# Kernel optimization log

Measured on AMD Instinct MI355X. Metric: run time of the kernel, lower is better.

## Reference

```python
import jax, jax.numpy as jnp
import numpy as np

B, N, C, H = 4, 1024, 1024, 16
HD = C // H  # 64
THETA = 10000.0


def _rope_cos_sin(n, hd, theta):
    # classic 1D RoPE cache; [n, hd] with each freq repeated twice (interleaved pairs)
    inv_freq = 1.0 / theta ** (jnp.arange(0, hd, 2, dtype=jnp.float32) / hd)
    t = jnp.arange(n, dtype=jnp.float32)
    freqs = t[:, None] * inv_freq[None, :]              # [n, hd/2]
    cos = jnp.repeat(jnp.cos(freqs), 2, axis=-1)        # [n, hd]
    sin = jnp.repeat(jnp.sin(freqs), 2, axis=-1)
    # original clones & forces row 0 to identity rotation (already true since t=0)
    cos = cos.at[0].set(1.0)
    sin = sin.at[0].set(0.0)
    return cos, sin


def _rotate_half(x):
    # interleaved rotate-half: (x0,x1,x2,x3,...) -> (-x1,x0,-x3,x2,...)
    x1 = x[..., 0::2]
    x2 = x[..., 1::2]
    return jnp.stack((-x2, x1), axis=-1).reshape(x.shape)


def setup_inputs() -> dict:
    key = jax.random.key(0)
    ks = jax.random.split(key, 5)
    s = 0.02
    return {
        "x": jax.random.normal(ks[0], (B, N, C), dtype=jnp.float32),
        "qkv_w": jax.random.normal(ks[1], (3 * C, C), dtype=jnp.float32) * s,
        "qkv_b": jax.random.normal(ks[2], (3 * C,), dtype=jnp.float32) * s,
        "proj_w": jax.random.normal(ks[3], (C, C), dtype=jnp.float32) * s,
        "proj_b": jax.random.normal(ks[4], (C,), dtype=jnp.float32) * s,
    }


def reference(x, qkv_w, qkv_b, proj_w, proj_b):
    b, n, c = x.shape
    h, hd = H, HD
    qkv = x @ qkv_w.T + qkv_b                              # [b, n, 3c]
    qkv = qkv.reshape(b, n, 3, h, hd).transpose(2, 0, 3, 1, 4)  # [3, b, h, n, hd]
    q, k, v = qkv[0], qkv[1], qkv[2]
    scale = hd ** -0.5
    q = q * scale                                          # explicit pre-scale (as in source)
    cos, sin = _rope_cos_sin(n, hd, THETA)                 # [n, hd]
    cos = cos[None, None]                                  # broadcast over b, h
    sin = sin[None, None]
    q = q * cos + _rotate_half(q) * sin
    k = k * cos + _rotate_half(k) * sin
    # F.scaled_dot_product_attention also applies its default 1/sqrt(hd) scale
    logits = jnp.einsum('bhqd,bhkd->bhqk', q, k) * scale   # [b, h, n, n]
    attn = jax.nn.softmax(logits, axis=-1)
    out = jnp.einsum('bhqk,bhkd->bhqd', attn, v)           # [b, h, n, hd]
    out = out.transpose(0, 2, 1, 3).reshape(b, n, c)
    return out @ proj_w.T + proj_b
```

## Files before the change

### kernel.cpp

```cpp
#include <hip/hip_runtime.h>
#include <hip/hip_bf16.h>
#include <stdint.h>

#define DEVI __device__ __forceinline__

typedef __attribute__((ext_vector_type(8))) short short8;
typedef __attribute__((ext_vector_type(4))) short short4v;
typedef __attribute__((ext_vector_type(4))) float floatx4;

DEVI ushort f2bf(float f) {
  union { float f; uint32_t u; } v; v.f = f;
  uint32_t u = v.u;
  uint32_t r = (u + 0x7FFFu + ((u >> 16) & 1u)) >> 16;
  return (ushort)r;
}
DEVI ushort f2bf_fast(float f) {
  union { float f; uint32_t u; } v; v.f = f;
  return (ushort)((v.u + 0x8000u) >> 16);
}
DEVI float bf2f(ushort h) {
  union { uint32_t u; float f; } v; v.u = ((uint32_t)h) << 16;
  return v.f;
}
DEVI void gld_lds16(const void* g, void* l) {
  __builtin_amdgcn_global_load_lds(
      (const __attribute__((address_space(1))) unsigned int*)g,
      (__attribute__((address_space(3))) unsigned int*)l, 16, 0, 0);
}

__global__ __launch_bounds__(256, 4) void cast_all(
    const float* __restrict__ x, const float* __restrict__ w1,
    const float* __restrict__ w2, ushort* __restrict__ xb,
    ushort* __restrict__ w1b, ushort* __restrict__ w2b,
    float2* __restrict__ tab) {
  const int N1 = 4096 * 1024, N2 = 3072 * 1024, N3 = 1024 * 1024;
  int id = blockIdx.x * 256 + threadIdx.x;
  if (id < 32768) {
    int j = id & 31, n = id >> 5;
    float inv = powf(10000.0f, -(float)(2 * j) / 64.0f);
    float fr = (float)n * inv;
    tab[id] = make_float2(cosf(fr), sinf(fr));
  }
  int i = id * 4;
  const int total = N1 + N2 + N3;
  int stride = gridDim.x * 256 * 4;
  for (; i < total; i += stride) {
    const float* src; ushort* dst; int off;
    if (i < N1) { src = x; dst = xb; off = i; }
    else if (i < N1 + N2) { src = w1; dst = w1b; off = i - N1; }
    else { src = w2; dst = w2b; off = i - N1 - N2; }
    float4 v = *(const float4*)(src + off);
    ushort4 o;
    o.x = f2bf(v.x); o.y = f2bf(v.y); o.z = f2bf(v.z); o.w = f2bf(v.w);
    *(ushort4*)(dst + off) = o;
  }
}

__global__ __launch_bounds__(256, 4) void gemm_qkv(
    const ushort* __restrict__ A, const ushort* __restrict__ Bm,
    const float* __restrict__ bias, const float2* __restrict__ tab,
    ushort* __restrict__ Qb, ushort* __restrict__ Kb,
    ushort* __restrict__ Vt) {
  __shared__ __align__(16) char pool[33792];
  char* AsP = pool;
  char* BsP = pool + 16384;
  const int tid = threadIdx.x;
  const int w = tid >> 6, lane = tid & 63;

  const int bid = blockIdx.x;
  const int xcd = bid & 7, i5 = bid >> 3;
  const int lm = i5 & 7, ln = i5 >> 3;
  const int mt = (xcd & 3) * 8 + lm;
  const int nt = (xcd >> 2) * 12 + ln;
  const int m0 = mt * 128, n0 = nt * 128;

  const int wm = (w >> 1) * 64, wn = (w & 1) * 64;
  const int lrow = lane & 15, g = lane >> 4;
  const int swrd = (g ^ ((lrow >> 1) & 3)) << 4;

  const int swsrc = (((lane & 3) ^ ((lane >> 3) & 3)) << 4);
  const char* aG = (const char*)A + (size_t)(m0 + w * 32 + (lane >> 2)) * 2048 + swsrc;
  const char* bG = (const char*)Bm + (size_t)(n0 + w * 32 + (lane >> 2)) * 2048 + swsrc;
  const int ldst = w * 2048 + lane * 16;

  auto STAGE = [&](const int buf) {
    gld_lds16(aG, AsP + buf * 8192 + ldst);
    gld_lds16(aG + 16 * 2048, AsP + buf * 8192 + ldst + 1024);
    gld_lds16(bG, BsP + buf * 8192 + ldst);
    gld_lds16(bG + 16 * 2048, BsP + buf * 8192 + ldst + 1024);
    aG += 64; bG += 64;
  };

  floatx4 acc[4][4] = {};

  auto TILE = [&](const int buf) {
    short8 af[4], bf[4];
#pragma unroll
    for (int t = 0; t < 4; ++t) {
      af[t] = *(const short8*)(AsP + buf * 8192 + (wm + t * 16 + lrow) * 64 + swrd);
      bf[t] = *(const short8*)(BsP + buf * 8192 + (wn + t * 16 + lrow) * 64 + swrd);
    }
#pragma unroll
    for (int i = 0; i < 4; ++i)
#pragma unroll
      for (int j = 0; j < 4; ++j)
        acc[i][j] = __builtin_amdgcn_mfma_f32_16x16x32_bf16(af[i], bf[j], acc[i][j], 0, 0, 0);
  };

  STAGE(0);
  asm volatile("s_waitcnt vmcnt(0)" ::: "memory");
  __builtin_amdgcn_s_barrier();
  __builtin_amdgcn_sched_barrier(0);

  for (int t = 0; t < 32; t += 2) {
    STAGE(1);
    __builtin_amdgcn_sched_barrier(0);
    TILE(0);
    asm volatile("s_waitcnt vmcnt(0)" ::: "memory");
    __builtin_amdgcn_s_barrier();
    __builtin_amdgcn_sched_barrier(0);

    if (t + 2 < 32) STAGE(0);
    __builtin_amdgcn_sched_barrier(0);
    TILE(1);
    asm volatile("s_waitcnt vmcnt(0)" ::: "memory");
    __builtin_amdgcn_s_barrier();
    __builtin_amdgcn_sched_barrier(0);
  }

  const int role = n0 >> 10;
  if (role == 2) {
    char* T = pool;
#pragma unroll
    for (int i = 0; i < 4; ++i) {
      int lr0 = wm + i * 16 + g * 4;
#pragma unroll
      for (int j = 0; j < 4; ++j) {
        int lc = wn + j * 16 + lrow;
        float bv = bias[n0 + lc];
        ushort4 o;
#pragma unroll
        for (int r = 0; r < 4; ++r) ((ushort*)&o)[r] = f2bf(acc[i][j][r] + bv);
        *(ushort4*)(T + lc * 264 + lr0 * 2) = o;
      }
    }
    __syncthreads();
    const int b = m0 >> 10, nbase = m0 & 1023;
    const int h0 = (n0 - 2048) >> 6;
    const int c = tid >> 1, half = tid & 1;
    const int h = h0 + (c >> 6), d = c & 63;
    ushort* dst = Vt + (size_t)(b * 16 + h) * 65536 + (size_t)d * 1024 + nbase + half * 64;
    const char* src = T + c * 264 + half * 128;
#pragma unroll
    for (int k = 0; k < 16; ++k)
      *(short4v*)(dst + k * 4) = *(const short4v*)(src + k * 8);
  } else {
    const float sc = (1.0f / 64.0f) * 1.44269504088896f;
#pragma unroll
    for (int i = 0; i < 4; ++i) {
      int mrow = m0 + wm + i * 16 + g * 4;
#pragma unroll
      for (int j = 0; j < 4; ++j) {
        int ncol = n0 + wn + j * 16 + lrow;
        float bv = bias[ncol];
        int cm = ncol & 1023;
        int h = cm >> 6, d = cm & 63;
#pragma unroll
        for (int r = 0; r < 4; ++r) {
          float v = acc[i][j][r] + bv;
          int row = mrow + r;
          int b = row >> 10, n = row & 1023;
          float p = __shfl_xor(v, 1);
          float2 cs = tab[n * 32 + (d >> 1)];
          float o = (d & 1) ? (v * cs.x + p * cs.y) : (v * cs.x - p * cs.y);
          if (role == 0) o *= sc;
          ushort* dstqk = (role == 0) ? Qb : Kb;
          dstqk[((size_t)(b * 16 + h) * 1024 + n) * 64 + d] = f2bf(o);
        }
      }
    }
  }
}

__global__ __launch_bounds__(256, 3) void gemm_proj(
    const ushort* __restrict__ A, const ushort* __restrict__ Bm,
    const float* __restrict__ bias, float* __restrict__ Cout) {
  __shared__ __align__(16) char lds[3][16384];
  char* L0 = &lds[0][0];
  const int tid = threadIdx.x;
  const int w = tid >> 6, lane = tid & 63;

  const int bid = blockIdx.x;
  const int xcd = bid & 7, i5 = bid >> 3;
  const int lm = i5 & 7, ln = i5 >> 3;
  const int mt = (xcd & 3) * 8 + lm;
  const int nt = (xcd >> 2) * 4 + ln;
  const int m0 = mt * 128, n0 = nt * 128;

  const int wm = (w >> 1) * 64, wn = (w & 1) * 64;
  const int lrow = lane & 15, g = lane >> 4;
  const int swrd = (g ^ ((lrow >> 1) & 3)) << 4;

  const int swsrc = (((lane & 3) ^ ((lane >> 3) & 3)) << 4);
  const char* aG = (const char*)A + (size_t)(m0 + w * 32 + (lane >> 2)) * 2048 + swsrc;
  const char* bG = (const char*)Bm + (size_t)(n0 + w * 32 + (lane >> 2)) * 2048 + swsrc;
  const int ldst = w * 2048 + lane * 16;

  auto STAGE = [&](const int base) {
    char* L = L0 + base;
    gld_lds16(aG, L + ldst);
    gld_lds16(aG + 16 * 2048, L + ldst + 1024);
    gld_lds16(bG, L + 8192 + ldst);
    gld_lds16(bG + 16 * 2048, L + 8192 + ldst + 1024);
    aG += 64; bG += 64;
  };

  floatx4 acc[4][4] = {};

  auto TILE = [&](const int base) {
    const char* L = L0 + base;
    short8 af[4], bf[4];
#pragma unroll
    for (int t = 0; t < 4; ++t) {
      af[t] = *(const short8*)(L + (wm + t * 16 + lrow) * 64 + swrd);
      bf[t] = *(const short8*)(L + 8192 + (wn + t * 16 + lrow) * 64 + swrd);
    }
#pragma unroll
    for (int i = 0; i < 4; ++i)
#pragma unroll
      for (int j = 0; j < 4; ++j)
        acc[i][j] = __builtin_amdgcn_mfma_f32_16x16x32_bf16(af[i], bf[j], acc[i][j], 0, 0, 0);
  };

  STAGE(0);
  STAGE(16384);
  int bT = 0, bS = 32768;

  for (int t = 0; t < 31; ++t) {
    asm volatile("s_waitcnt vmcnt(4)" ::: "memory");
    __builtin_amdgcn_s_barrier();
    __builtin_amdgcn_sched_barrier(0);
    if (t < 30) STAGE(bS);
    __builtin_amdgcn_sched_barrier(0);
    TILE(bT);
    __builtin_amdgcn_sched_barrier(0);
    bT += 16384; if (bT == 49152) bT = 0;
    bS += 16384; if (bS == 49152) bS = 0;
  }
  asm volatile("s_waitcnt vmcnt(0)" ::: "memory");
  __builtin_amdgcn_s_barrier();
  __builtin_amdgcn_sched_barrier(0);
  TILE(bT);

#pragma unroll
  for (int i = 0; i < 4; ++i) {
    int mrow = m0 + wm + i * 16 + (lane >> 4) * 4;
#pragma unroll
    for (int j = 0; j < 4; ++j) {
      int ncol = n0 + wn + j * 16 + (lane & 15);
      float bv = bias[ncol];
#pragma unroll
      for (int r = 0; r < 4; ++r)
        Cout[(size_t)(mrow + r) * 1024 + ncol] = acc[i][j][r] + bv;
    }
  }
}

__global__ __launch_bounds__(256, 4) void attn(
    const ushort* __restrict__ Q, const ushort* __restrict__ Kc,
    const ushort* __restrict__ Vt, ushort* __restrict__ AO) {
  __shared__ char lds[2][16384];
  char* ldsbase = &lds[0][0];
  int id = blockIdx.x;
  int bh = id & 63, qi = id >> 6;
  int b = bh >> 4, h = bh & 15;
  int q0 = qi * 64;
  int tid = threadIdx.x, w = tid >> 6, lane = tid & 63;
  int l15 = lane & 15, g = lane >> 4;
  const ushort* Qbh = Q + (size_t)bh * 65536;
  const char* Kbh = (const char*)(Kc + (size_t)bh * 65536);
  const char* Vbh = (const char*)(Vt + (size_t)bh * 65536);

  short8 qf[2];
#pragma unroll
  for (int ks = 0; ks < 2; ++ks)
    qf[ks] = *(const short8*)(Qbh + (size_t)(q0 + w * 16 + l15) * 64 + ks * 32 + g * 8);

  int kaddr[8];
#pragma unroll
  for (int ks = 0; ks < 2; ++ks)
#pragma unroll
    for (int nt = 0; nt < 4; ++nt) {
      int row = nt * 16 + l15;
      kaddr[ks * 4 + nt] = (row * 128 + ks * 64 + g * 16) ^ ((row & 7) << 4);
    }
  int vaddr[16];
#pragma unroll
  for (int ch = 0; ch < 2; ++ch)
#pragma unroll
    for (int dt = 0; dt < 4; ++dt)
#pragma unroll
      for (int hf = 0; hf < 2; ++hf) {
        int row = dt * 16 + l15;
        vaddr[(ch * 4 + dt) * 2 + hf] =
            8192 + ((row * 128 + ch * 64 + hf * 32 + g * 8) ^ ((row & 7) << 4));
      }

  const int d0 = w * 2048 + lane * 16;
  const int d1 = d0 + 1024;
  const int r0 = d0 >> 7, r1 = d1 >> 7;
  const int s0 = d0 ^ ((r0 & 7) << 4), s1 = d1 ^ ((r1 & 7) << 4);
  const char* pK0 = Kbh + s0;
  const char* pK1 = Kbh + s1;
  const char* pV0 = Vbh + r0 * 2048 + (s0 & 127);
  const char* pV1 = Vbh + r1 * 2048 + (s1 & 127);

  auto STAGE = [&](const int B) {
    gld_lds16(pK0, ldsbase + B + d0);
    gld_lds16(pK1, ldsbase + B + d1);
    gld_lds16(pV0, ldsbase + B + 8192 + d0);
    gld_lds16(pV1, ldsbase + B + 8192 + d1);
    pK0 += 8192; pK1 += 8192; pV0 += 128; pV1 += 128;
  };

  floatx4 oacc[4] = {};
  float lrun = 0.f;

  auto TILE = [&](const int B) {
    floatx4 sacc[4] = {};
    __builtin_amdgcn_s_setprio(1);
#pragma unroll
    for (int ks = 0; ks < 2; ++ks) {
      short8 kf[4];
#pragma unroll
      for (int nt = 0; nt < 4; ++nt)
        kf[nt] = *(const short8*)(ldsbase + B + kaddr[ks * 4 + nt]);
#pragma unroll
      for (int nt = 0; nt < 4; ++nt)
        sacc[nt] = __builtin_amdgcn_mfma_f32_16x16x32_bf16(kf[nt], qf[ks], sacc[nt], 0, 0, 0);
    }
    __builtin_amdgcn_s_setprio(0);

    float rs = 0.f;
#pragma unroll
    for (int nt = 0; nt < 4; ++nt)
#pragma unroll
      for (int r = 0; r < 4; ++r) {
        float p = __builtin_amdgcn_exp2f(sacc[nt][r]);
        sacc[nt][r] = p;
        rs += p;
      }
    lrun += rs;

    short8 pa[2];
#pragma unroll
    for (int ch = 0; ch < 2; ++ch)
#pragma unroll
      for (int r = 0; r < 4; ++r) {
        pa[ch][r] = (short)f2bf_fast(sacc[2 * ch][r]);
        pa[ch][r + 4] = (short)f2bf_fast(sacc[2 * ch + 1][r]);
      }

    __builtin_amdgcn_s_setprio(1);
#pragma unroll
    for (int ch = 0; ch < 2; ++ch)
#pragma unroll
      for (int dt = 0; dt < 4; ++dt) {
        short4v va = *(const short4v*)(ldsbase + B + vaddr[(ch * 4 + dt) * 2]);
        short4v vb = *(const short4v*)(ldsbase + B + vaddr[(ch * 4 + dt) * 2 + 1]);
        short8 vf = __builtin_shufflevector(va, vb, 0, 1, 2, 3, 4, 5, 6, 7);
        oacc[dt] = __builtin_amdgcn_mfma_f32_16x16x32_bf16(pa[ch], vf, oacc[dt], 0, 0, 0);
      }
    __builtin_amdgcn_s_setprio(0);
  };

  STAGE(0);
  asm volatile("s_waitcnt vmcnt(0)" ::: "memory");
  __builtin_amdgcn_s_barrier();
  __builtin_amdgcn_sched_barrier(0);

  for (int kt = 0; kt < 16; kt += 2) {
    STAGE(16384);
    __builtin_amdgcn_sched_barrier(0);
    TILE(0);
    asm volatile("s_waitcnt vmcnt(0)" ::: "memory");
    __builtin_amdgcn_s_barrier();
    __builtin_amdgcn_sched_barrier(0);

    if (kt + 2 < 16) STAGE(0);
    __builtin_amdgcn_sched_barrier(0);
    TILE(16384);
    asm volatile("s_waitcnt vmcnt(0)" ::: "memory");
    __builtin_amdgcn_s_barrier();
    __builtin_amdgcn_sched_barrier(0);
  }

  lrun += __shfl_xor(lrun, 16);
  lrun += __shfl_xor(lrun, 32);
  float linv = 1.0f / lrun;
  float linvR[4];
#pragma unroll
  for (int r = 0; r < 4; ++r) linvR[r] = __shfl(linv, g * 4 + r);
#pragma unroll
  for (int r = 0; r < 4; ++r) {
    int nseq = q0 + w * 16 + g * 4 + r;
#pragma unroll
    for (int dt = 0; dt < 4; ++dt) {
      int d = dt * 16 + l15;
      AO[(size_t)(b * 1024 + nseq) * 1024 + h * 64 + d] = f2bf(oacc[dt][r] * linvR[r]);
    }
  }
}

extern "C" void kernel_launch(void* const* d_in, const int* in_sizes, int n_in,
                              void* d_out, int out_size, void* d_ws, size_t ws_size,
                              hipStream_t stream) {
  const float* x = (const float*)d_in[0];
  const float* qkv_w = (const float*)d_in[1];
  const float* qkv_b = (const float*)d_in[2];
  const float* proj_w = (const float*)d_in[3];
  const float* proj_b = (const float*)d_in[4];
  float* out = (float*)d_out;

  char* ws = (char*)d_ws;
  size_t off = 0;
  auto alloc = [&](size_t bytes) -> void* {
    void* p = ws + off;
    off += (bytes + 255) & ~(size_t)255;
    return p;
  };
  ushort* xb = (ushort*)alloc(4096ull * 1024 * 2);
  ushort* wqkvb = (ushort*)alloc(3072ull * 1024 * 2);
  ushort* wprojb = (ushort*)alloc(1024ull * 1024 * 2);
  ushort* Qb = (ushort*)alloc(64ull * 1024 * 64 * 2);
  ushort* Kb = (ushort*)alloc(64ull * 1024 * 64 * 2);
  ushort* Vt = (ushort*)alloc(64ull * 1024 * 64 * 2);
  ushort* AO = (ushort*)alloc(4096ull * 1024 * 2);
  float2* tab = (float2*)alloc(1024ull * 32 * sizeof(float2));

  cast_all<<<2048, 256, 0, stream>>>(x, qkv_w, proj_w, xb, wqkvb, wprojb, tab);

  gemm_qkv<<<768, 256, 0, stream>>>(xb, wqkvb, qkv_b, tab, Qb, Kb, Vt);

  attn<<<1024, 256, 0, stream>>>(Qb, Kb, Vt, AO);

  gemm_proj<<<256, 256, 0, stream>>>(AO, wprojb, proj_b, out);
}
```

Baseline: 86.02 us.

## Stage Q/K epilogue through LDS and double query rows per attention block

The Q/K epilogue of the QKV GEMM now writes rotated results into a padded LDS tile and then emits contiguous 16-byte stores per row, replacing the scattered 2-byte global stores. The attention kernel now handles 128 query rows per block instead of 64, so each K/V tile staged in LDS feeds twice as many MFMAs, and it launches half as many blocks. The aim is to cut redundant K/V global traffic and uncoalesced stores. In exchange it raises register pressure from doubled accumulators and the preloaded K fragments, and it lowers the block count, which may hurt occupancy.

```diff
diff --git a/kernel.cpp b/kernel.cpp
--- a/kernel.cpp
+++ b/kernel.cpp
@@ -61,7 +61,7 @@
     const float* __restrict__ bias, const float2* __restrict__ tab,
     ushort* __restrict__ Qb, ushort* __restrict__ Kb,
     ushort* __restrict__ Vt) {
-  __shared__ __align__(16) char pool[33792];
+  __shared__ __align__(16) char pool[34816];
   char* AsP = pool;
   char* BsP = pool + 16384;
   const int tid = threadIdx.x;
@@ -129,6 +129,7 @@
   }
 
   const int role = n0 >> 10;
+  const int b = m0 >> 10, nbase = m0 & 1023;
   if (role == 2) {
     char* T = pool;
 #pragma unroll
@@ -145,7 +146,6 @@
       }
     }
     __syncthreads();
-    const int b = m0 >> 10, nbase = m0 & 1023;
     const int h0 = (n0 - 2048) >> 6;
     const int c = tid >> 1, half = tid & 1;
     const int h = h0 + (c >> 6), d = c & 63;
@@ -156,29 +156,37 @@
       *(short4v*)(dst + k * 4) = *(const short4v*)(src + k * 8);
   } else {
     const float sc = (1.0f / 64.0f) * 1.44269504088896f;
+    char* T = pool;
 #pragma unroll
     for (int i = 0; i < 4; ++i) {
-      int mrow = m0 + wm + i * 16 + g * 4;
+      int lr0 = wm + i * 16 + g * 4;
 #pragma unroll
       for (int j = 0; j < 4; ++j) {
-        int ncol = n0 + wn + j * 16 + lrow;
+        int lc = wn + j * 16 + lrow;
+        int ncol = n0 + lc;
         float bv = bias[ncol];
-        int cm = ncol & 1023;
-        int h = cm >> 6, d = cm & 63;
+        int d = ncol & 63;
 #pragma unroll
         for (int r = 0; r < 4; ++r) {
           float v = acc[i][j][r] + bv;
-          int row = mrow + r;
-          int b = row >> 10, n = row & 1023;
+          int n = (nbase + lr0 + r);
           float p = __shfl_xor(v, 1);
           float2 cs = tab[n * 32 + (d >> 1)];
           float o = (d & 1) ? (v * cs.x + p * cs.y) : (v * cs.x - p * cs.y);
           if (role == 0) o *= sc;
-          ushort* dstqk = (role == 0) ? Qb : Kb;
-          dstqk[((size_t)(b * 16 + h) * 1024 + n) * 64 + d] = f2bf(o);
+          *(ushort*)(T + (lr0 + r) * 272 + lc * 2) = f2bf(o);
         }
       }
     }
+    __syncthreads();
+    const int h0 = (n0 & 1023) >> 6;
+    const int n_l = tid >> 1, half = tid & 1;
+    ushort* dst = (role == 0 ? Qb : Kb) +
+                  (size_t)(b * 16 + h0 + half) * 65536 + (size_t)(nbase + n_l) * 64;
+    const char* src = T + n_l * 272 + half * 128;
+#pragma unroll
+    for (int k = 0; k < 8; ++k)
+      *(short8*)(dst + k * 8) = *(const short8*)(src + k * 16);
   }
 }
 
@@ -274,17 +282,19 @@
   int id = blockIdx.x;
   int bh = id & 63, qi = id >> 6;
   int b = bh >> 4, h = bh & 15;
-  int q0 = qi * 64;
+  int q0 = qi * 128;
   int tid = threadIdx.x, w = tid >> 6, lane = tid & 63;
   int l15 = lane & 15, g = lane >> 4;
   const ushort* Qbh = Q + (size_t)bh * 65536;
   const char* Kbh = (const char*)(Kc + (size_t)bh * 65536);
   const char* Vbh = (const char*)(Vt + (size_t)bh * 65536);
 
-  short8 qf[2];
-#pragma unroll
-  for (int ks = 0; ks < 2; ++ks)
-    qf[ks] = *(const short8*)(Qbh + (size_t)(q0 + w * 16 + l15) * 64 + ks * 32 + g * 8);
+  short8 qf[2][2];
+#pragma unroll
+  for (int hh = 0; hh < 2; ++hh)
+#pragma unroll
+    for (int ks = 0; ks < 2; ++ks)
+      qf[hh][ks] = *(const short8*)(Qbh + (size_t)(q0 + hh * 64 + w * 16 + l15) * 64 + ks * 32 + g * 8);
 
   int kaddr[8];
 #pragma unroll
@@ -323,43 +333,45 @@
     pK0 += 8192; pK1 += 8192; pV0 += 128; pV1 += 128;
   };
 
-  floatx4 oacc[4] = {};
-  float lrun = 0.f;
+  floatx4 oacc[2][4] = {};
+  float lrun[2] = {0.f, 0.f};
 
   auto TILE = [&](const int B) {
-    floatx4 sacc[4] = {};
-    __builtin_amdgcn_s_setprio(1);
-#pragma unroll
-    for (int ks = 0; ks < 2; ++ks) {
-      short8 kf[4];
+    short8 kf[8];
+#pragma unroll
+    for (int t = 0; t < 8; ++t)
+      kf[t] = *(const short8*)(ldsbase + B + kaddr[t]);
+
+    short8 pa[2][2];
+#pragma unroll
+    for (int hh = 0; hh < 2; ++hh) {
+      floatx4 sacc[4] = {};
+      __builtin_amdgcn_s_setprio(1);
+#pragma unroll
+      for (int ks = 0; ks < 2; ++ks)
+#pragma unroll
+        for (int nt = 0; nt < 4; ++nt)
+          sacc[nt] = __builtin_amdgcn_mfma_f32_16x16x32_bf16(kf[ks * 4 + nt], qf[hh][ks], sacc[nt], 0, 0, 0);
+      __builtin_amdgcn_s_setprio(0);
+
+      float rs = 0.f;
 #pragma unroll
       for (int nt = 0; nt < 4; ++nt)
-        kf[nt] = *(const short8*)(ldsbase + B + kaddr[ks * 4 + nt]);
-#pragma unroll
-      for (int nt = 0; nt < 4; ++nt)
-        sacc[nt] = __builtin_amdgcn_mfma_f32_16x16x32_bf16(kf[nt], qf[ks], sacc[nt], 0, 0, 0);
-    }
-    __builtin_amdgcn_s_setprio(0);
-
-    float rs = 0.f;
-#pragma unroll
-    for (int nt = 0; nt < 4; ++nt)
-#pragma unroll
-      for (int r = 0; r < 4; ++r) {
-        float p = __builtin_amdgcn_exp2f(sacc[nt][r]);
-        sacc[nt][r] = p;
-        rs += p;
-      }
-    lrun += rs;
-
-    short8 pa[2];
-#pragma unroll
-    for (int ch = 0; ch < 2; ++ch)
-#pragma unroll
-      for (int r = 0; r < 4; ++r) {
-        pa[ch][r] = (short)f2bf_fast(sacc[2 * ch][r]);
-        pa[ch][r + 4] = (short)f2bf_fast(sacc[2 * ch + 1][r]);
-      }
+#pragma unroll
+        for (int r = 0; r < 4; ++r) {
+          float p = __builtin_amdgcn_exp2f(sacc[nt][r]);
+          sacc[nt][r] = p;
+          rs += p;
+        }
+      lrun[hh] += rs;
+#pragma unroll
+      for (int ch = 0; ch < 2; ++ch)
+#pragma unroll
+        for (int r = 0; r < 4; ++r) {
+          pa[hh][ch][r] = (short)f2bf_fast(sacc[2 * ch][r]);
+          pa[hh][ch][r + 4] = (short)f2bf_fast(sacc[2 * ch + 1][r]);
+        }
+    }
 
     __builtin_amdgcn_s_setprio(1);
 #pragma unroll
@@ -369,7 +381,9 @@
         short4v va = *(const short4v*)(ldsbase + B + vaddr[(ch * 4 + dt) * 2]);
         short4v vb = *(const short4v*)(ldsbase + B + vaddr[(ch * 4 + dt) * 2 + 1]);
         short8 vf = __builtin_shufflevector(va, vb, 0, 1, 2, 3, 4, 5, 6, 7);
-        oacc[dt] = __builtin_amdgcn_mfma_f32_16x16x32_bf16(pa[ch], vf, oacc[dt], 0, 0, 0);
+#pragma unroll
+        for (int hh = 0; hh < 2; ++hh)
+          oacc[hh][dt] = __builtin_amdgcn_mfma_f32_16x16x32_bf16(pa[hh][ch], vf, oacc[hh][dt], 0, 0, 0);
       }
     __builtin_amdgcn_s_setprio(0);
   };
@@ -395,19 +409,23 @@
     __builtin_amdgcn_sched_barrier(0);
   }
 
-  lrun += __shfl_xor(lrun, 16);
-  lrun += __shfl_xor(lrun, 32);
-  float linv = 1.0f / lrun;
-  float linvR[4];
-#pragma unroll
-  for (int r = 0; r < 4; ++r) linvR[r] = __shfl(linv, g * 4 + r);
-#pragma unroll
-  for (int r = 0; r < 4; ++r) {
-    int nseq = q0 + w * 16 + g * 4 + r;
-#pragma unroll
-    for (int dt = 0; dt < 4; ++dt) {
-      int d = dt * 16 + l15;
-      AO[(size_t)(b * 1024 + nseq) * 1024 + h * 64 + d] = f2bf(oacc[dt][r] * linvR[r]);
+#pragma unroll
+  for (int hh = 0; hh < 2; ++hh) {
+    float l = lrun[hh];
+    l += __shfl_xor(l, 16);
+    l += __shfl_xor(l, 32);
+    float linv = 1.0f / l;
+    float linvR[4];
+#pragma unroll
+    for (int r = 0; r < 4; ++r) linvR[r] = __shfl(linv, g * 4 + r);
+#pragma unroll
+    for (int r = 0; r < 4; ++r) {
+      int nseq = q0 + hh * 64 + w * 16 + g * 4 + r;
+#pragma unroll
+      for (int dt = 0; dt < 4; ++dt) {
+        int d = dt * 16 + l15;
+        AO[(size_t)(b * 1024 + nseq) * 1024 + h * 64 + d] = f2bf(oacc[hh][dt][r] * linvR[r]);
+      }
     }
   }
 }
@@ -442,7 +460,7 @@
 
   gemm_qkv<<<768, 256, 0, stream>>>(xb, wqkvb, qkv_b, tab, Qb, Kb, Vt);
 
-  attn<<<1024, 256, 0, stream>>>(Qb, Kb, Vt, AO);
+  attn<<<512, 256, 0, stream>>>(Qb, Kb, Vt, AO);
 
   gemm_proj<<<256, 256, 0, stream>>>(AO, wprojb, proj_b, out);
 }
```

After: 146.6 us. 1.7x slower.
